# Kernel tuning notes

Measured on AMD Instinct MI355X. Metric: run time of the kernel, lower is better.

Reference implementation:

```python
import jax, jax.numpy as jnp
import numpy as np

N_TOK, TOKDIM = 2048, 1024
NHEADS, KDIM = 16, 64


def setup_inputs() -> dict:
    key = jax.random.key(0)
    kg, kk, kq = jax.random.split(key, 3)
    g = jax.random.normal(kg, (N_TOK, TOKDIM), dtype=jnp.float32)
    # params use normal(stddev=0.002) init, as in the flax module
    Wk = 0.002 * jax.random.normal(kk, (NHEADS, KDIM, TOKDIM), dtype=jnp.float32)
    Wq = 0.002 * jax.random.normal(kq, (NHEADS, KDIM, TOKDIM), dtype=jnp.float32)
    return {"g": g, "Wk": Wk, "Wq": Wq}


def reference(g, Wk, Wq):
    """manual_grad of the attention energy: returns d(energy)/dg, shape [n, d]."""
    H, Z, D = Wk.shape
    betas = jnp.full((H,), 1.0, dtype=g.dtype) / jnp.sqrt(jnp.asarray(Z, g.dtype))
    K = jnp.einsum('hzd,kd->khz', Wk, g)   # [n,h,z]
    Q = jnp.einsum('hzd,qd->qhz', Wq, g)   # [n,h,z]
    F1 = jnp.einsum('hzd,khz->khd', Wq, K)  # [n,h,d]
    F2 = jnp.einsum('hzd,qhz->qhd', Wk, Q)  # [n,h,d]
    A1 = jnp.einsum('h,khz,qhz->hqk', betas, K, Q)  # [h,q,k] scores
    A2 = jax.nn.softmax(A1, -1)
    T1 = -jnp.einsum('khd,hqk->qd', F1, A2)
    T2 = -jnp.einsum('qhd,hqk->kd', F2, A2)
    return T1 + T2
```

## Files before the change

### kernel.cpp

```cpp
#include <hip/hip_runtime.h>
#include <stdint.h>

#define NT 2048
#define TD 1024
#define NH 16
static constexpr float SCL = 0.18033688011112042f;

typedef __attribute__((ext_vector_type(8))) short bf16x8;
typedef __attribute__((ext_vector_type(4))) float f32x4;
typedef __attribute__((ext_vector_type(16))) float f32x16;
typedef __attribute__((address_space(3))) uint32_t lds_u32;
typedef __attribute__((address_space(1))) uint32_t glb_u32;

__device__ __forceinline__ float bf2f(unsigned short u){
  union { uint32_t u32; float f; } v; v.u32 = ((uint32_t)u) << 16; return v.f;
}
__device__ __forceinline__ unsigned short f2bf(float f){
  union { float f; uint32_t u; } v; v.f = f;
  uint32_t r = v.u + 0x7fffu + ((v.u >> 16) & 1u);
  return (unsigned short)(r >> 16);
}
__device__ __forceinline__ bf16x8 ld8(const unsigned short* base, int row, int kc){
  return *(const bf16x8*)((const char*)base + row*128 + ((kc ^ (row & 7)) << 4));
}
template<int N> __device__ __forceinline__ void wait_vm_lgkm0(){
  if constexpr (N == 0)      asm volatile("s_waitcnt vmcnt(0) lgkmcnt(0)" ::: "memory");
  else if constexpr (N == 4) asm volatile("s_waitcnt vmcnt(4) lgkmcnt(0)" ::: "memory");
  else if constexpr (N == 6) asm volatile("s_waitcnt vmcnt(6) lgkmcnt(0)" ::: "memory");
  __builtin_amdgcn_sched_barrier(0);
}

__global__ __launch_bounds__(256) void prep_kernel(
    const float* __restrict__ g, const float* __restrict__ Wk, const float* __restrict__ Wq,
    unsigned short* __restrict__ gbf, unsigned short* __restrict__ wkq,
    unsigned short* __restrict__ twqk)
{
  int b = blockIdx.x;
  if (b < 1024) {
    int base = b * 2048 + threadIdx.x;
    #pragma unroll
    for (int i = 0; i < 8; i++) { int idx = base + i * 256; gbf[idx] = f2bf(g[idx]); }
  } else if (b < 2048) {
    int base = (b - 1024) * 2048 + threadIdx.x;
    #pragma unroll
    for (int i = 0; i < 8; i++) {
      int idx = base + i * 256;
      float v = (idx < (1 << 20)) ? Wk[idx] : Wq[idx - (1 << 20)];
      wkq[idx] = f2bf(v);
    }
  } else {
    int t = b - 2048;
    int dt = t & 31, jt = t >> 5;
    __shared__ float tile[32][33];
    int tx = threadIdx.x & 31, ty = threadIdx.x >> 5;
    int j0 = jt * 32, d0 = dt * 32;
    const float* src = (j0 < 1024) ? Wq : Wk;
    int jb = (j0 < 1024) ? j0 : (j0 - 1024);
    #pragma unroll
    for (int rr = 0; rr < 4; rr++)
      tile[ty + rr * 8][tx] = src[(size_t)(jb + ty + rr * 8) * 1024 + d0 + tx];
    __syncthreads();
    #pragma unroll
    for (int rr = 0; rr < 4; rr++)
      twqk[(size_t)(d0 + ty + rr * 8) * 2048 + j0 + tx] = f2bf(tile[tx][ty + rr * 8]);
  }
}

__global__ __launch_bounds__(256) void pack_pck(const unsigned short* __restrict__ CKQ,
                                                unsigned short* __restrict__ PCK)
{
  int tile = blockIdx.x;
  int cb = tile >> 6, rb = tile & 63;
  __shared__ unsigned short t[32][72];
  int tid = threadIdx.x;
  int r = tid >> 3, c0 = (tid & 7) * 8;
  const unsigned short* src = CKQ + (size_t)(rb * 32 + r) * 2048 + cb * 64 + c0;
  *(ushort4*)&t[r][c0]     = *(const ushort4*)src;
  *(ushort4*)&t[r][c0 + 4] = *(const ushort4*)(src + 4);
  __syncthreads();
  int kz = tid >> 6, l = tid & 63;
  int zl = kz * 16 + 8 * (l >> 5);
  ushort4 lo = *(ushort4*)&t[l & 31][zl];
  ushort4 hi4 = *(ushort4*)&t[l & 31][zl + 4];
  unsigned short* dst = PCK + ((size_t)(tile * 4 + kz) * 64 + l) * 8;
  *(ushort4*)dst       = lo;
  *(ushort4*)(dst + 4) = hi4;
}

template<bool DIVL>
__global__ __launch_bounds__(256) void pack_pbx(const unsigned short* __restrict__ CKQ,
                                                const float* __restrict__ L,
                                                unsigned short* __restrict__ PBX)
{
  int bid = blockIdx.x;
  int qb = bid & 63, hz = bid >> 6;
  int h = hz >> 1, zb = hz & 1;
  int colbase = (DIVL ? 1024 : 0) + h * 64 + zb * 32;
  __shared__ unsigned short tq[32][36];
  __shared__ float rcpL[32];
  int tid = threadIdx.x;
  int r = tid >> 3, c0 = (tid & 7) * 4;
  *(ushort4*)&tq[r][c0] =
      *(const ushort4*)(CKQ + (size_t)(qb * 32 + r) * 2048 + colbase + c0);
  if (DIVL && tid < 32) rcpL[tid] = 1.0f / L[(size_t)h * NT + qb * 32 + tid];
  __syncthreads();
  if (tid < 128) {
    int ks = tid >> 6, l = tid & 63;
    int zl = l & 31, hi = l >> 5;
    unsigned short ob[8];
    #pragma unroll
    for (int e = 0; e < 8; e++) {
      int ql = 16 * ks + 8 * (e >> 2) + 4 * hi + (e & 3);
      unsigned short v = tq[ql][zl];
      if (DIVL) v = f2bf(bf2f(v) * rcpL[ql]);
      ob[e] = v;
    }
    unsigned short* dst = PBX + ((size_t)(bid * 2 + ks) * 64 + l) * 8;
    *(ushort4*)dst       = *(ushort4*)&ob[0];
    *(ushort4*)(dst + 4) = *(ushort4*)&ob[4];
  }
}

template<int TM, int TN, int EPI, int WPE>
__global__ __launch_bounds__(256, WPE) void btg2_kernel(
    const unsigned short* __restrict__ A, int lda,
    const unsigned short* __restrict__ BT, int ldb,
    int Kdim, void* C0)
{
  constexpr int WM = TM / 2, WN = TN / 2, FM = WM / 16, FN = WN / 16;
  constexpr int AC = TM / 32, BC = TN / 32, LOADS = AC + BC;
  __shared__ __align__(16) unsigned short As[3][TM * 64];
  __shared__ __align__(16) unsigned short Bs[3][TN * 64];
  int tid = threadIdx.x, lane = tid & 63, wave = tid >> 6;
  int wr = wave >> 1, wc = wave & 1, lrow = lane & 15, g = lane >> 4;
  int bm = blockIdx.x * TM, bn = blockIdx.y * TN;

  auto stage = [&](unsigned short* bufA, unsigned short* bufB, int kk) {
    #pragma unroll
    for (int i = 0; i < AC; i++) {
      int c = i * 256 + tid, row = c >> 3, sl = ((c & 7) ^ (row & 7)) << 3;
      __builtin_amdgcn_global_load_lds((glb_u32*)(A + (size_t)(bm + row) * lda + kk + sl),
          (lds_u32*)((char*)bufA + i * 4096 + wave * 1024), 16, 0, 0);
    }
    #pragma unroll
    for (int i = 0; i < BC; i++) {
      int c = i * 256 + tid, row = c >> 3, sl = ((c & 7) ^ (row & 7)) << 3;
      __builtin_amdgcn_global_load_lds((glb_u32*)(BT + (size_t)(bn + row) * ldb + kk + sl),
          (lds_u32*)((char*)bufB + i * 4096 + wave * 1024), 16, 0, 0);
    }
  };

  f32x4 acc[FM][FN] = {};
  int nt = Kdim >> 6;
  stage(As[0], Bs[0], 0);
  stage(As[1], Bs[1], 64);
  wait_vm_lgkm0<LOADS>();
  __builtin_amdgcn_s_barrier();
  int bc = 0;
  for (int t = 0; t < nt; t++) {
    int bp = bc + 2; if (bp >= 3) bp -= 3;
    if (t + 2 < nt) stage(As[bp], Bs[bp], (t + 2) * 64);
    const unsigned short* Ac = As[bc];
    const unsigned short* Bc = Bs[bc];
    #pragma unroll
    for (int k2 = 0; k2 < 2; k2++) {
      bf16x8 a_[FM], b_[FN];
      #pragma unroll
      for (int m = 0; m < FM; m++) a_[m] = ld8(Ac, wr * WM + m * 16 + lrow, k2 * 4 + g);
      #pragma unroll
      for (int n = 0; n < FN; n++) b_[n] = ld8(Bc, wc * WN + n * 16 + lrow, k2 * 4 + g);
      #pragma unroll
      for (int m = 0; m < FM; m++)
        #pragma unroll
        for (int n = 0; n < FN; n++)
          acc[m][n] = __builtin_amdgcn_mfma_f32_16x16x32_bf16(a_[m], b_[n], acc[m][n], 0, 0, 0);
    }
    if (t + 2 < nt) wait_vm_lgkm0<LOADS>(); else wait_vm_lgkm0<0>();
    __builtin_amdgcn_s_barrier();
    bc = (bc == 2) ? 0 : bc + 1;
  }
  #pragma unroll
  for (int m = 0; m < FM; m++) {
    int rb = bm + wr * WM + m * 16 + 4 * g;
    #pragma unroll
    for (int n = 0; n < FN; n++) {
      int cc = bn + wc * WN + n * 16 + lrow;
      f32x4 v = acc[m][n];
      if constexpr (EPI == 0) {
        unsigned short* Cp = (unsigned short*)C0;
        #pragma unroll
        for (int j = 0; j < 4; j++) Cp[(size_t)(rb + j) * 2048 + cc] = f2bf(v[j]);
      } else {
        float* Cf = (float*)C0;
        #pragma unroll
        for (int j = 0; j < 4; j++) Cf[(size_t)(rb + j) * 1024 + cc] = -v[j];
      }
    }
  }
}

template<bool DIV>
__global__ __launch_bounds__(256, 2) void fused_kernel(
    const unsigned short* __restrict__ PCK,
    const unsigned short* __restrict__ PBX,
    unsigned short* __restrict__ C,
    float* __restrict__ Lg)
{
  __shared__ __align__(16) float Red[2][64][68];
  __shared__ float L_lds[64];
  int tid = threadIdx.x, l = tid & 63, w = tid >> 6;
  int zr = l & 31, hi = l >> 5;
  int lin = blockIdx.x;
  int wgid = (lin & 7) * 64 + (lin >> 3);
  int h = wgid >> 5, pB = wgid & 31, p0 = pB * 64;
  int cbA = DIV ? h : 16 + h;
  int cbB = DIV ? 16 + h : h;
  const bf16x8* PCKf = (const bf16x8*)PCK;
  const bf16x8* PBXf = (const bf16x8*)PBX;

  bf16x8 bs[2][4];
  #pragma unroll
  for (int ps = 0; ps < 2; ps++)
    #pragma unroll
    for (int kz = 0; kz < 4; kz++)
      bs[ps][kz] = PCKf[((size_t)(cbB * 64 + pB * 2 + ps) * 4 + kz) * 64 + l];

  auto load = [&](bf16x8 (&a_)[4], bf16x8 (&pb_)[2][2], int rb){
    #pragma unroll
    for (int kz = 0; kz < 4; kz++)
      a_[kz] = PCKf[((size_t)(cbA * 64 + rb) * 4 + kz) * 64 + l];
    #pragma unroll
    for (int zb = 0; zb < 2; zb++)
      #pragma unroll
      for (int ks = 0; ks < 2; ks++)
        pb_[zb][ks] = PBXf[((size_t)((h * 2 + zb) * 64 + rb) * 2 + ks) * 64 + l];
  };

  f32x16 acc_pv[2][2] = {};
  float lsum[2] = {0.f, 0.f};
  bf16x8 a_c[4], pb_c[2][2];
  load(a_c, pb_c, w * 16);

  for (int t = 0; t < 16; t++) {
    bf16x8 a_n[4], pb_n[2][2];
    if (t + 1 < 16) load(a_n, pb_n, w * 16 + t + 1);
    f32x16 acc_s[2] = {};
    #pragma unroll
    for (int kz = 0; kz < 4; kz++) {
      acc_s[0] = __builtin_amdgcn_mfma_f32_32x32x16_bf16(a_c[kz], bs[0][kz], acc_s[0], 0, 0, 0);
      acc_s[1] = __builtin_amdgcn_mfma_f32_32x32x16_bf16(a_c[kz], bs[1][kz], acc_s[1], 0, 0, 0);
    }
    union { bf16x8 v; uint32_t u[4]; } pu[2][2];
    #pragma unroll
    for (int ps = 0; ps < 2; ps++) {
      float ev[16];
      #pragma unroll
      for (int r = 0; r < 16; r++) ev[r] = exp2f(acc_s[ps][r] * SCL);
      if (DIV) {
        #pragma unroll
        for (int r = 0; r < 16; r++) lsum[ps] += ev[r];
      }
      #pragma unroll
      for (int ks = 0; ks < 2; ks++)
        #pragma unroll
        for (int i = 0; i < 4; i++)
          asm("v_cvt_pk_bf16_f32 %0, %1, %2"
              : "=v"(pu[ps][ks].u[i]) : "v"(ev[8 * ks + 2 * i]), "v"(ev[8 * ks + 2 * i + 1]));
    }
    #pragma unroll
    for (int zb = 0; zb < 2; zb++)
      #pragma unroll
      for (int ks = 0; ks < 2; ks++) {
        acc_pv[0][zb] = __builtin_amdgcn_mfma_f32_32x32x16_bf16(pu[0][ks].v, pb_c[zb][ks], acc_pv[0][zb], 0, 0, 0);
        acc_pv[1][zb] = __builtin_amdgcn_mfma_f32_32x32x16_bf16(pu[1][ks].v, pb_c[zb][ks], acc_pv[1][zb], 0, 0, 0);
      }
    #pragma unroll
    for (int kz = 0; kz < 4; kz++) a_c[kz] = a_n[kz];
    #pragma unroll
    for (int zb = 0; zb < 2; zb++)
      #pragma unroll
      for (int ks = 0; ks < 2; ks++) pb_c[zb][ks] = pb_n[zb][ks];
  }

  if (w >= 2) {
    #pragma unroll
    for (int ps = 0; ps < 2; ps++)
      #pragma unroll
      for (int zb = 0; zb < 2; zb++) {
        int z = zb * 32 + zr;
        #pragma unroll
        for (int u = 0; u < 4; u++) {
          int p = ps * 32 + 8 * u + 4 * hi;
          f32x4 q;
          q[0] = acc_pv[ps][zb][4 * u];     q[1] = acc_pv[ps][zb][4 * u + 1];
          q[2] = acc_pv[ps][zb][4 * u + 2]; q[3] = acc_pv[ps][zb][4 * u + 3];
          *(f32x4*)&Red[w - 2][z][p] = q;
        }
      }
  }
  if (DIV && tid < 64) L_lds[tid] = 0.f;
  __syncthreads();
  if (w < 2) {
    #pragma unroll
    for (int ps = 0; ps < 2; ps++)
      #pragma unroll
      for (int zb = 0; zb < 2; zb++) {
        int z = zb * 32 + zr;
        #pragma unroll
        for (int u = 0; u < 4; u++) {
          int p = ps * 32 + 8 * u + 4 * hi;
          float* slot = &Red[w][z][p];
          f32x4 q = *(f32x4*)slot;
          q[0] += acc_pv[ps][zb][4 * u];     q[1] += acc_pv[ps][zb][4 * u + 1];
          q[2] += acc_pv[ps][zb][4 * u + 2]; q[3] += acc_pv[ps][zb][4 * u + 3];
          *(f32x4*)slot = q;
        }
      }
  }
  if (DIV) {
    #pragma unroll
    for (int ps = 0; ps < 2; ps++) {
      float s = lsum[ps];
      s += __shfl_xor(s, 32);
      if (hi == 0) atomicAdd(&L_lds[ps * 32 + zr], s);
    }
  }
  __syncthreads();
  if (DIV && tid < 64) Lg[(size_t)h * NT + p0 + tid] = L_lds[tid];
  int p = tid >> 2, z16 = (tid & 3) * 16;
  float inv = DIV ? 1.0f / L_lds[p] : 1.0f;
  int cbase = DIV ? h * 64 : TD + h * 64;
  unsigned short ob[16];
  #pragma unroll
  for (int i = 0; i < 16; i++) {
    int z = z16 + i;
    float x = Red[0][z][p] + Red[1][z][p];
    ob[i] = f2bf(x * inv);
  }
  unsigned short* dst = C + (size_t)(p0 + p) * 2048 + cbase + z16;
  *(ushort4*)dst        = *(ushort4*)&ob[0];
  *(ushort4*)(dst + 4)  = *(ushort4*)&ob[4];
  *(ushort4*)(dst + 8)  = *(ushort4*)&ob[8];
  *(ushort4*)(dst + 12) = *(ushort4*)&ob[12];
}

extern "C" void kernel_launch(void* const* d_in, const int* in_sizes, int n_in,
                              void* d_out, int out_size, void* d_ws, size_t ws_size,
                              hipStream_t stream)
{
  (void)in_sizes; (void)n_in; (void)out_size; (void)ws_size;
  const float* g  = (const float*)d_in[0];
  const float* Wk = (const float*)d_in[1];
  const float* Wq = (const float*)d_in[2];

  char* ws = (char*)d_ws;
  size_t off = 0;
  auto alloc = [&](size_t b) -> char* {
    char* p = ws + off; off += (b + 255) & ~((size_t)255); return p;
  };
  unsigned short* gbf  = (unsigned short*)alloc((size_t)NT * TD * 2);
  unsigned short* wkq  = (unsigned short*)alloc((size_t)2 * TD * TD * 2);
  unsigned short* twqk = (unsigned short*)alloc((size_t)TD * 2048 * 2);
  unsigned short* CKQ  = (unsigned short*)alloc((size_t)NT * 2048 * 2);
  unsigned short* PCK  = (unsigned short*)alloc((size_t)NT * 2048 * 2);
  unsigned short* PBT  = (unsigned short*)alloc((size_t)TD * NT * 2);
  unsigned short* QSTP = (unsigned short*)alloc((size_t)TD * NT * 2);
  unsigned short* CB12 = (unsigned short*)alloc((size_t)NT * 2048 * 2);
  float*          Lbuf = (float*)alloc((size_t)NH * NT * 4);

  prep_kernel<<<dim3(4096), dim3(256), 0, stream>>>(g, Wk, Wq, gbf, wkq, twqk);

  btg2_kernel<128, 64, 0, 2><<<dim3(16, 32), dim3(256), 0, stream>>>(
      gbf, TD, wkq, TD, TD, (void*)CKQ);

  pack_pck<<<dim3(2048), dim3(256), 0, stream>>>(CKQ, PCK);
  pack_pbx<false><<<dim3(2048), dim3(256), 0, stream>>>(CKQ, nullptr, PBT);

  fused_kernel<true><<<dim3(512), dim3(256), 0, stream>>>(PCK, PBT, CB12, Lbuf);

  pack_pbx<true><<<dim3(2048), dim3(256), 0, stream>>>(CKQ, Lbuf, QSTP);

  fused_kernel<false><<<dim3(512), dim3(256), 0, stream>>>(PCK, QSTP, CB12, nullptr);

  btg2_kernel<128, 64, 4, 2><<<dim3(16, 16), dim3(256), 0, stream>>>(
      CB12, 2048, twqk, 2048, 2048, d_out);
}
```

Before: 117.6 us.

## Replace final LDS-tiled GEMM with MFMA-fragment-packed out_kernel

The attention outputs and the transposed weight matrix are now written directly in a packed MFMA-fragment layout: fused_kernel emits it from its epilogue and prep_kernel emits it from its transpose path. A new out_kernel then loads operands straight from global memory into registers with a one-step prefetch. It splits the reduction dimension across four waves and combines the partial sums through LDS, replacing the generic btg2 GEMM with its LDS staging and barriers. The trade-off is no LDS reuse, so each wave reads its operands straight from global and L2, and there is an added cross-wave reduction.

```diff
diff --git a/kernel.cpp b/kernel.cpp
--- a/kernel.cpp
+++ b/kernel.cpp
@@ -33,7 +33,7 @@
 __global__ __launch_bounds__(256) void prep_kernel(
     const float* __restrict__ g, const float* __restrict__ Wk, const float* __restrict__ Wq,
     unsigned short* __restrict__ gbf, unsigned short* __restrict__ wkq,
-    unsigned short* __restrict__ twqk)
+    unsigned short* __restrict__ TWP)
 {
   int b = blockIdx.x;
   if (b < 1024) {
@@ -50,19 +50,30 @@
     }
   } else {
     int t = b - 2048;
-    int dt = t & 31, jt = t >> 5;
-    __shared__ float tile[32][33];
-    int tx = threadIdx.x & 31, ty = threadIdx.x >> 5;
-    int j0 = jt * 32, d0 = dt * 32;
+    int db = t & 31, jzg = t >> 5;
+    int d0 = db * 32, j0 = jzg * 128;
+    __shared__ unsigned short tile[128][33];
+    int tid = threadIdx.x;
     const float* src = (j0 < 1024) ? Wq : Wk;
     int jb = (j0 < 1024) ? j0 : (j0 - 1024);
     #pragma unroll
-    for (int rr = 0; rr < 4; rr++)
-      tile[ty + rr * 8][tx] = src[(size_t)(jb + ty + rr * 8) * 1024 + d0 + tx];
+    for (int i = 0; i < 16; i++) {
+      int idx = i * 256 + tid, r = idx >> 5, c = idx & 31;
+      tile[r][c] = f2bf(src[(size_t)(jb + r) * 1024 + d0 + c]);
+    }
     __syncthreads();
-    #pragma unroll
-    for (int rr = 0; rr < 4; rr++)
-      twqk[(size_t)(d0 + ty + rr * 8) * 2048 + j0 + tx] = f2bf(tile[tx][ty + rr * 8]);
+    int jq = tid >> 6, l = tid & 63;
+    #pragma unroll
+    for (int f = 0; f < 2; f++) {
+      int jzl = jq * 2 + f;
+      unsigned short ob[8];
+      #pragma unroll
+      for (int e = 0; e < 8; e++)
+        ob[e] = tile[jzl * 16 + 8 * (l >> 5) + e][l & 31];
+      unsigned short* dst = TWP + ((size_t)(db * 128 + jzg * 8 + jzl) * 64 + l) * 8;
+      *(ushort4*)dst       = *(ushort4*)&ob[0];
+      *(ushort4*)(dst + 4) = *(ushort4*)&ob[4];
+    }
   }
 }
 
@@ -186,15 +197,9 @@
     for (int n = 0; n < FN; n++) {
       int cc = bn + wc * WN + n * 16 + lrow;
       f32x4 v = acc[m][n];
-      if constexpr (EPI == 0) {
-        unsigned short* Cp = (unsigned short*)C0;
-        #pragma unroll
-        for (int j = 0; j < 4; j++) Cp[(size_t)(rb + j) * 2048 + cc] = f2bf(v[j]);
-      } else {
-        float* Cf = (float*)C0;
-        #pragma unroll
-        for (int j = 0; j < 4; j++) Cf[(size_t)(rb + j) * 1024 + cc] = -v[j];
-      }
+      unsigned short* Cp = (unsigned short*)C0;
+      #pragma unroll
+      for (int j = 0; j < 4; j++) Cp[(size_t)(rb + j) * 2048 + cc] = f2bf(v[j]);
     }
   }
 }
@@ -203,7 +208,7 @@
 __global__ __launch_bounds__(256, 2) void fused_kernel(
     const unsigned short* __restrict__ PCK,
     const unsigned short* __restrict__ PBX,
-    unsigned short* __restrict__ C,
+    unsigned short* __restrict__ PA,
     float* __restrict__ Lg)
 {
   __shared__ __align__(16) float Red[2][64][68];
@@ -330,6 +335,8 @@
   int p = tid >> 2, z16 = (tid & 3) * 16;
   float inv = DIV ? 1.0f / L_lds[p] : 1.0f;
   int cbase = DIV ? h * 64 : TD + h * 64;
+  int jz = (cbase + z16) >> 4;
+  int tok = p0 + p, tb = tok >> 5, tl = tok & 31;
   unsigned short ob[16];
   #pragma unroll
   for (int i = 0; i < 16; i++) {
@@ -337,11 +344,94 @@
     float x = Red[0][z][p] + Red[1][z][p];
     ob[i] = f2bf(x * inv);
   }
-  unsigned short* dst = C + (size_t)(p0 + p) * 2048 + cbase + z16;
-  *(ushort4*)dst        = *(ushort4*)&ob[0];
-  *(ushort4*)(dst + 4)  = *(ushort4*)&ob[4];
-  *(ushort4*)(dst + 8)  = *(ushort4*)&ob[8];
-  *(ushort4*)(dst + 12) = *(ushort4*)&ob[12];
+  unsigned short* dst = PA + (((size_t)jz * 64 + tb) * 64) * 8;
+  *(ushort4*)(dst + tl * 8)            = *(ushort4*)&ob[0];
+  *(ushort4*)(dst + tl * 8 + 4)        = *(ushort4*)&ob[4];
+  *(ushort4*)(dst + (32 + tl) * 8)     = *(ushort4*)&ob[8];
+  *(ushort4*)(dst + (32 + tl) * 8 + 4) = *(ushort4*)&ob[12];
+}
+
+__global__ __launch_bounds__(256, 2) void out_kernel(
+    const unsigned short* __restrict__ PA,
+    const unsigned short* __restrict__ TWP,
+    float* __restrict__ out)
+{
+  __shared__ __align__(16) float Red[2][64][68];
+  int tid = threadIdx.x, l = tid & 63, w = tid >> 6;
+  int zr = l & 31, hi = l >> 5;
+  int lin = blockIdx.x;
+  int wgid = (lin & 7) * 64 + (lin >> 3);
+  int tokb = wgid >> 4, db2 = wgid & 15;
+  const bf16x8* PAf = (const bf16x8*)PA;
+  const bf16x8* TWf = (const bf16x8*)TWP;
+
+  f32x16 acc[2][2] = {};
+  bf16x8 a_c[2], b_c[2];
+  auto loadx = [&](bf16x8 (&a_)[2], bf16x8 (&b_)[2], int jz){
+    #pragma unroll
+    for (int th = 0; th < 2; th++)
+      a_[th] = PAf[((size_t)jz * 64 + tokb * 2 + th) * 64 + l];
+    #pragma unroll
+    for (int dh = 0; dh < 2; dh++)
+      b_[dh] = TWf[((size_t)(db2 * 2 + dh) * 128 + jz) * 64 + l];
+  };
+  loadx(a_c, b_c, w * 32);
+  for (int it = 0; it < 32; it++) {
+    bf16x8 a_n[2], b_n[2];
+    if (it + 1 < 32) loadx(a_n, b_n, w * 32 + it + 1);
+    #pragma unroll
+    for (int th = 0; th < 2; th++)
+      #pragma unroll
+      for (int dh = 0; dh < 2; dh++)
+        acc[th][dh] = __builtin_amdgcn_mfma_f32_32x32x16_bf16(a_c[th], b_c[dh], acc[th][dh], 0, 0, 0);
+    #pragma unroll
+    for (int i = 0; i < 2; i++) { a_c[i] = a_n[i]; b_c[i] = b_n[i]; }
+  }
+  if (w >= 2) {
+    #pragma unroll
+    for (int th = 0; th < 2; th++)
+      #pragma unroll
+      for (int dh = 0; dh < 2; dh++) {
+        int d = dh * 32 + zr;
+        #pragma unroll
+        for (int u = 0; u < 4; u++) {
+          int tk = th * 32 + 8 * u + 4 * hi;
+          f32x4 q;
+          q[0] = acc[th][dh][4 * u];     q[1] = acc[th][dh][4 * u + 1];
+          q[2] = acc[th][dh][4 * u + 2]; q[3] = acc[th][dh][4 * u + 3];
+          *(f32x4*)&Red[w - 2][d][tk] = q;
+        }
+      }
+  }
+  __syncthreads();
+  if (w < 2) {
+    #pragma unroll
+    for (int th = 0; th < 2; th++)
+      #pragma unroll
+      for (int dh = 0; dh < 2; dh++) {
+        int d = dh * 32 + zr;
+        #pragma unroll
+        for (int u = 0; u < 4; u++) {
+          int tk = th * 32 + 8 * u + 4 * hi;
+          float* slot = &Red[w][d][tk];
+          f32x4 q = *(f32x4*)slot;
+          q[0] += acc[th][dh][4 * u];     q[1] += acc[th][dh][4 * u + 1];
+          q[2] += acc[th][dh][4 * u + 2]; q[3] += acc[th][dh][4 * u + 3];
+          *(f32x4*)slot = q;
+        }
+      }
+  }
+  __syncthreads();
+  int p = tid >> 2, d16 = (tid & 3) * 16;
+  float* dst = out + (size_t)(tokb * 64 + p) * 1024 + db2 * 64 + d16;
+  #pragma unroll
+  for (int i4 = 0; i4 < 16; i4 += 4) {
+    f32x4 r;
+    #pragma unroll
+    for (int j = 0; j < 4; j++)
+      r[j] = -(Red[0][d16 + i4 + j][p] + Red[1][d16 + i4 + j][p]);
+    *(f32x4*)(dst + i4) = r;
+  }
 }
 
 extern "C" void kernel_launch(void* const* d_in, const int* in_sizes, int n_in,
@@ -360,15 +450,15 @@
   };
   unsigned short* gbf  = (unsigned short*)alloc((size_t)NT * TD * 2);
   unsigned short* wkq  = (unsigned short*)alloc((size_t)2 * TD * TD * 2);
-  unsigned short* twqk = (unsigned short*)alloc((size_t)TD * 2048 * 2);
+  unsigned short* TWP  = (unsigned short*)alloc((size_t)TD * 2048 * 2);
   unsigned short* CKQ  = (unsigned short*)alloc((size_t)NT * 2048 * 2);
   unsigned short* PCK  = (unsigned short*)alloc((size_t)NT * 2048 * 2);
   unsigned short* PBT  = (unsigned short*)alloc((size_t)TD * NT * 2);
   unsigned short* QSTP = (unsigned short*)alloc((size_t)TD * NT * 2);
-  unsigned short* CB12 = (unsigned short*)alloc((size_t)NT * 2048 * 2);
+  unsigned short* PA   = (unsigned short*)alloc((size_t)NT * 2048 * 2);
   float*          Lbuf = (float*)alloc((size_t)NH * NT * 4);
 
-  prep_kernel<<<dim3(4096), dim3(256), 0, stream>>>(g, Wk, Wq, gbf, wkq, twqk);
+  prep_kernel<<<dim3(2560), dim3(256), 0, stream>>>(g, Wk, Wq, gbf, wkq, TWP);
 
   btg2_kernel<128, 64, 0, 2><<<dim3(16, 32), dim3(256), 0, stream>>>(
       gbf, TD, wkq, TD, TD, (void*)CKQ);
@@ -376,12 +466,11 @@
   pack_pck<<<dim3(2048), dim3(256), 0, stream>>>(CKQ, PCK);
   pack_pbx<false><<<dim3(2048), dim3(256), 0, stream>>>(CKQ, nullptr, PBT);
 
-  fused_kernel<true><<<dim3(512), dim3(256), 0, stream>>>(PCK, PBT, CB12, Lbuf);
+  fused_kernel<true><<<dim3(512), dim3(256), 0, stream>>>(PCK, PBT, PA, Lbuf);
 
   pack_pbx<true><<<dim3(2048), dim3(256), 0, stream>>>(CKQ, Lbuf, QSTP);
 
-  fused_kernel<false><<<dim3(512), dim3(256), 0, stream>>>(PCK, QSTP, CB12, nullptr);
-
-  btg2_kernel<128, 64, 4, 2><<<dim3(16, 16), dim3(256), 0, stream>>>(
-      CB12, 2048, twqk, 2048, 2048, d_out);
-}
+  fused_kernel<false><<<dim3(512), dim3(256), 0, stream>>>(PCK, QSTP, PA, nullptr);
+
+  out_kernel<<<dim3(512), dim3(256), 0, stream>>>(PA, TWP, (float*)d_out);
+}
```

After: 107.1 us. 1.1x faster.
